# Optimization experiments

Measured on AMD Instinct MI355X. Metric: run time of the kernel, lower is better.

## Reference

```python
import jax, jax.numpy as jnp
import numpy as np
from math import sqrt

BATCH = 32
NUM_CLASSES = 81   # incl. background (class 0 skipped)
MAX_DET = 200      # max_output / per-class NMS candidate cap
IOU_T = 0.5        # criteria in decode_batch_with_nms_trace
CONF_T = 0.05      # score mask threshold


def make_dboxes():
    """Replicates dboxes_R34_coco([1200,1200]) -> (15130, 4) xywh, clipped to [0,1]."""
    fig = 1200
    feat = [50, 25, 13, 7, 3, 3]
    scales = [int(s * fig / 300) for s in [21, 45, 99, 153, 207, 261, 315]]
    ars = [[2], [2, 3], [2, 3], [2, 3], [2], [2]]
    boxes = []
    for idx, f in enumerate(feat):
        sk1 = scales[idx] / fig
        sk2 = scales[idx + 1] / fig
        sk3 = sqrt(sk1 * sk2)
        sizes = [(sk1, sk1), (sk3, sk3)]
        for a in ars[idx]:
            w, h = sk1 * sqrt(a), sk1 / sqrt(a)
            sizes += [(w, h), (h, w)]
        fk = fig // (fig // f)
        for (w, h) in sizes:
            for i in range(f):
                for j in range(f):
                    boxes.append(((j + 0.5) / fk, (i + 0.5) / fk, w, h))
    return np.clip(np.asarray(boxes, np.float32), 0.0, 1.0)


def setup_inputs() -> dict:
    key = jax.random.key(0)
    k1, k2 = jax.random.split(key)
    db = make_dboxes()                      # (15130, 4)
    N = db.shape[0]
    return {
        "bboxes_in": jax.random.normal(k1, (BATCH, 4, N), jnp.float32),
        "scores_in": jax.random.normal(k2, (BATCH, NUM_CLASSES, N), jnp.float32),
        "scale_xy": jnp.full((1,), 0.1, jnp.float32),
        "scale_wh": jnp.full((1,), 0.2, jnp.float32),
        "dboxes_xywh": jnp.asarray(db)[None],  # (1, N, 4)
    }


def _scale_back(bboxes_in, scores_in, scale_xy, scale_wh, dboxes_xywh):
    bb = jnp.transpose(bboxes_in, (0, 2, 1))          # (B, N, 4)
    sc = jnp.transpose(scores_in, (0, 2, 1))          # (B, N, L)
    d_xy, d_wh = dboxes_xywh[..., :2], dboxes_xywh[..., 2:]
    xy = bb[..., :2] * scale_xy * d_wh + d_xy
    wh = jnp.exp(bb[..., 2:] * scale_wh) * d_wh
    ltrb = jnp.concatenate([xy - 0.5 * wh, xy + 0.5 * wh], axis=-1)
    return ltrb, jax.nn.softmax(sc, axis=-1)


def _pairwise_iou(a, b):
    lt = jnp.maximum(a[:, None, :2], b[None, :, :2])
    rb = jnp.minimum(a[:, None, 2:], b[None, :, 2:])
    wh = jnp.clip(rb - lt, 0.0)
    inter = wh[..., 0] * wh[..., 1]
    area_a = (a[:, 2] - a[:, 0]) * (a[:, 3] - a[:, 1])
    area_b = (b[:, 2] - b[:, 0]) * (b[:, 3] - b[:, 1])
    return inter / (area_a[:, None] + area_b[None, :] - inter)


def _nms_one_class(boxes, cls_scores):
    """boxes (N,4), cls_scores (N,) -> (MAX_DET,4), (MAX_DET,) with suppressed = -1."""
    s = jnp.where(cls_scores > CONF_T, cls_scores, -1.0)   # mask score > 0.05
    top_s, idx = jax.lax.top_k(s, MAX_DET)                 # descending topk
    b = boxes[idx]
    iou = _pairwise_iou(b, b)                              # (K, K)
    valid = top_s > CONF_T

    def body(i, keep):  # greedy NMS over score-sorted candidates
        sup = (iou[i] > IOU_T) & keep[i] & (jnp.arange(MAX_DET) > i)
        return keep & ~sup

    keep = jax.lax.stop_gradient(jax.lax.fori_loop(0, MAX_DET, body, valid))
    return b, jnp.where(keep, top_s, -1.0)


def _decode(bboxes_in, scores_in, scale_xy, scale_wh, dboxes_xywh):
    boxes, probs = _scale_back(bboxes_in, scores_in, scale_xy, scale_wh, dboxes_xywh)
    cls_scores = jnp.transpose(probs[..., 1:], (0, 2, 1))   # (B, C=80, N); skip bg
    B, C = cls_scores.shape[0], cls_scores.shape[1]
    per_class = jax.vmap(_nms_one_class, in_axes=(None, 0))
    kb, ks = jax.vmap(per_class, in_axes=(0, 0))(boxes, cls_scores)  # (B,C,K,4),(B,C,K)
    labels = jnp.broadcast_to(
        jnp.arange(1, C + 1, dtype=jnp.int32)[:, None], (C, MAX_DET)).reshape(-1)
    kb = kb.reshape(B, C * MAX_DET, 4)
    ks = ks.reshape(B, C * MAX_DET)
    top_s, top_i = jax.lax.top_k(ks, MAX_DET)               # global top-200
    fb = jnp.take_along_axis(kb, top_i[..., None], axis=1)  # (B, 200, 4)
    fl = labels[top_i]                                      # (B, 200)
    valid = top_s > CONF_T
    return (fb * valid[..., None].astype(fb.dtype),
            jnp.where(valid, fl, 0),
            jnp.where(valid, top_s, 0.0))


def reference(bboxes_in, scores_in, scale_xy, scale_wh, dboxes_xywh):
    return _decode(bboxes_in, scores_in, scale_xy, scale_wh, dboxes_xywh)
```

## Files before the change

### kernel.cpp

```cpp
#include <hip/hip_runtime.h>
#include <stdint.h>

#define NPRIOR   15130
#define BATCH    32
#define NCLS     81
#define NCLS_OUT 80
#define NDET     200
#define CONF_T   0.05f
#define IOU_T    0.5f
#define CAND_CAP 1024
#define NGRP     5
#define GRP      16
#define NCNT     (BATCH * NCLS_OUT)

__global__ __launch_bounds__(256, 1) void decode_softmax_scatter(
    const float* __restrict__ bboxes,
    const float* __restrict__ scores,
    const float* __restrict__ scale_xy_p,
    const float* __restrict__ scale_wh_p,
    const float* __restrict__ dboxes,
    float* __restrict__ boxes_ltrb,
    unsigned int* __restrict__ counters,
    unsigned long long* __restrict__ cand_g)
{
    int b = blockIdx.y;
    int n = blockIdx.x * 256 + threadIdx.x;
    if (n >= NPRIOR) return;

    float sx = scale_xy_p[0], sw = scale_wh_p[0];
    const float* bb = bboxes + (size_t)b * 4 * NPRIOR + n;
    float bx = bb[0];
    float by = bb[NPRIOR];
    float bw = bb[2 * NPRIOR];
    float bh = bb[3 * NPRIOR];
    float4 d = ((const float4*)dboxes)[n];
    float x = __fadd_rn(__fmul_rn(__fmul_rn(bx, sx), d.z), d.x);
    float y = __fadd_rn(__fmul_rn(__fmul_rn(by, sx), d.w), d.y);
    float w = __fmul_rn(expf(__fmul_rn(bw, sw)), d.z);
    float h = __fmul_rn(expf(__fmul_rn(bh, sw)), d.w);
    float hw = __fmul_rn(0.5f, w), hh = __fmul_rn(0.5f, h);
    float4 box;
    box.x = __fsub_rn(x, hw);
    box.y = __fsub_rn(y, hh);
    box.z = __fadd_rn(x, hw);
    box.w = __fadd_rn(y, hh);
    ((float4*)boxes_ltrb)[(size_t)b * NPRIOR + n] = box;

    const float* sc = scores + (size_t)b * NCLS * NPRIOR + n;
    float v[NCLS];
    float mx = -INFINITY;
#pragma unroll
    for (int c = 0; c < NCLS; ++c) {
        v[c] = sc[(size_t)c * NPRIOR];
        mx = fmaxf(mx, v[c]);
    }
    float sum = 0.f;
#pragma unroll
    for (int c = 0; c < NCLS; ++c) {
        v[c] = expf(__fsub_rn(v[c], mx));
        sum = __fadd_rn(sum, v[c]);
    }

    unsigned int invn = 0xFFFFFFFFu - (unsigned int)n;
    unsigned int cbase = (unsigned int)b * NCLS_OUT;
#pragma unroll
    for (int c = 1; c < NCLS; ++c) {
        float p = __fdiv_rn(v[c], sum);
        if (p > CONF_T) {
            unsigned int idx = cbase + (unsigned int)(c - 1);
            unsigned int pos = atomicAdd(&counters[idx], 1u);
            if (pos < CAND_CAP) {
                cand_g[(size_t)idx * CAND_CAP + pos] =
                    ((unsigned long long)__float_as_uint(p) << 32) | (unsigned long long)invn;
            }
        }
    }
}

__device__ inline void bitonic_desc(unsigned long long* keys, int P, int tid) {
    for (int k = 2; k <= P; k <<= 1) {
        for (int j = k >> 1; j > 0; j >>= 1) {
            for (int i = tid; i < P; i += 256) {
                int l = i ^ j;
                if (l > i) {
                    unsigned long long a = keys[i], b = keys[l];
                    bool desc = ((i & k) == 0);
                    if (desc ? (a < b) : (a > b)) {
                        keys[i] = b;
                        keys[l] = a;
                    }
                }
            }
            __syncthreads();
        }
    }
}

__global__ __launch_bounds__(256) void nms_class(
    const unsigned int* __restrict__ counters,
    const unsigned long long* __restrict__ cand_g,
    const float* __restrict__ boxes_ltrb,
    float* __restrict__ cls_scores,
    float* __restrict__ cls_boxes)
{
    __shared__ unsigned long long cand[CAND_CAP];
    __shared__ float sbox[NDET][4];
    __shared__ float sscore[NDET];
    __shared__ unsigned long long rowm[NDET][4];
    __shared__ unsigned long long keepw[4];

    int tid = threadIdx.x;
    int b = blockIdx.y;
    int bc = b * NCLS_OUT + blockIdx.x;

    unsigned int cntu = counters[bc];
    int cnt = (cntu > CAND_CAP) ? CAND_CAP : (int)cntu;

    int P = 256;
    while (P < cnt) P <<= 1;

    for (int i = tid; i < P; i += 256)
        cand[i] = (i < cnt) ? cand_g[(size_t)bc * CAND_CAP + i] : 0ull;
    __syncthreads();

    bitonic_desc(cand, P, tid);

    int m = cnt < NDET ? cnt : NDET;
    if (tid < m) {
        unsigned long long key = cand[tid];
        unsigned int n = 0xFFFFFFFFu - (unsigned int)(key & 0xFFFFFFFFull);
        sscore[tid] = __uint_as_float((unsigned int)(key >> 32));
        float4 bx = ((const float4*)boxes_ltrb)[(size_t)b * NPRIOR + n];
        sbox[tid][0] = bx.x;
        sbox[tid][1] = bx.y;
        sbox[tid][2] = bx.z;
        sbox[tid][3] = bx.w;
    }
    __syncthreads();

    if (tid < m) {
        float l0 = sbox[tid][0], t0 = sbox[tid][1], r0 = sbox[tid][2], b0 = sbox[tid][3];
        float area0 = __fmul_rn(__fsub_rn(r0, l0), __fsub_rn(b0, t0));
        unsigned long long w0 = 0, w1 = 0, w2 = 0, w3 = 0;
        for (int j = tid + 1; j < m; ++j) {
            float lj = sbox[j][0], tj = sbox[j][1], rj = sbox[j][2], bj = sbox[j][3];
            float ltx = fmaxf(l0, lj), lty = fmaxf(t0, tj);
            float rbx = fminf(r0, rj), rby = fminf(b0, bj);
            float iw = fmaxf(__fsub_rn(rbx, ltx), 0.f);
            float ih = fmaxf(__fsub_rn(rby, lty), 0.f);
            float inter = __fmul_rn(iw, ih);
            float areaj = __fmul_rn(__fsub_rn(rj, lj), __fsub_rn(bj, tj));
            float den = __fsub_rn(__fadd_rn(area0, areaj), inter);
            float iou = __fdiv_rn(inter, den);
            if (iou > IOU_T) {
                if (j < 64) w0 |= 1ull << j;
                else if (j < 128) w1 |= 1ull << (j - 64);
                else if (j < 192) w2 |= 1ull << (j - 128);
                else w3 |= 1ull << (j - 192);
            }
        }
        rowm[tid][0] = w0;
        rowm[tid][1] = w1;
        rowm[tid][2] = w2;
        rowm[tid][3] = w3;
    }
    __syncthreads();

    if (tid == 0) {
        auto maskf = [](int t) -> unsigned long long {
            if (t <= 0) return 0ull;
            if (t >= 64) return ~0ull;
            return (1ull << t) - 1ull;
        };
        unsigned long long k0 = maskf(m), k1 = maskf(m - 64), k2 = maskf(m - 128), k3 = maskf(m - 192);
#pragma unroll 4
        for (int i = 0; i < m; ++i) {
            unsigned long long r0 = rowm[i][0], r1 = rowm[i][1];
            unsigned long long r2 = rowm[i][2], r3 = rowm[i][3];
            unsigned long long cur = (i < 64) ? k0 : (i < 128) ? k1 : (i < 192) ? k2 : k3;
            if ((cur >> (i & 63)) & 1ull) {
                k0 &= ~r0; k1 &= ~r1; k2 &= ~r2; k3 &= ~r3;
            }
        }
        keepw[0] = k0; keepw[1] = k1; keepw[2] = k2; keepw[3] = k3;
    }
    __syncthreads();

    if (tid < NDET) {
        float s = -1.0f;
        if (tid < m && ((keepw[tid >> 6] >> (tid & 63)) & 1ull)) s = sscore[tid];
        cls_scores[(size_t)bc * NDET + tid] = s;
        if (tid < m) {
            float4 bx;
            bx.x = sbox[tid][0]; bx.y = sbox[tid][1];
            bx.z = sbox[tid][2]; bx.w = sbox[tid][3];
            ((float4*)cls_boxes)[(size_t)bc * NDET + tid] = bx;
        }
    }
}

__global__ __launch_bounds__(256) void topk_group(
    const float* __restrict__ cls_scores,
    unsigned long long* __restrict__ grp_keys)
{
    __shared__ unsigned long long keys[4096];
    __shared__ unsigned int cnt_s;

    int tid = threadIdx.x;
    int g = blockIdx.x, b = blockIdx.y;
    if (tid == 0) cnt_s = 0;
    __syncthreads();

    int base_e = g * GRP * NDET;
    const float* sp = cls_scores + (size_t)b * NCLS_OUT * NDET + base_e;
    for (int i = tid; i < GRP * NDET; i += 256) {
        float s = sp[i];
        if (s > CONF_T) {
            unsigned int pos = atomicAdd(&cnt_s, 1u);
            unsigned int e = (unsigned int)(base_e + i);
            keys[pos] = ((unsigned long long)__float_as_uint(s) << 32) |
                        (unsigned long long)(0xFFFFFFFFu - e);
        }
    }
    __syncthreads();
    int cnt = (int)cnt_s;
    int P = 256;
    while (P < cnt) P <<= 1;
    for (int i = tid; i < P; i += 256)
        if (i >= cnt) keys[i] = 0ull;
    __syncthreads();

    bitonic_desc(keys, P, tid);

    if (tid < NDET)
        grp_keys[((size_t)b * NGRP + g) * NDET + tid] = (tid < cnt) ? keys[tid] : 0ull;
}

__global__ __launch_bounds__(256) void final_topk(
    const unsigned long long* __restrict__ grp_keys,
    const float* __restrict__ cls_boxes,
    float* __restrict__ out)
{
    __shared__ unsigned long long keys[1024];
    __shared__ unsigned int cnt_s;

    int tid = threadIdx.x, b = blockIdx.x;
    if (tid == 0) cnt_s = 0;
    __syncthreads();

    for (int i = tid; i < NGRP * NDET; i += 256) {
        unsigned long long k = grp_keys[(size_t)b * NGRP * NDET + i];
        if (k != 0ull) keys[atomicAdd(&cnt_s, 1u)] = k;
    }
    __syncthreads();
    int cnt = (int)cnt_s;
    int P = 256;
    while (P < cnt) P <<= 1;
    for (int i = tid; i < P; i += 256)
        if (i >= cnt) keys[i] = 0ull;
    __syncthreads();

    bitonic_desc(keys, P, tid);

    if (tid < NDET) {
        float4 bx = make_float4(0.f, 0.f, 0.f, 0.f);
        float lab = 0.f, sc = 0.f;
        if (tid < cnt) {
            unsigned long long k = keys[tid];
            unsigned int e = 0xFFFFFFFFu - (unsigned int)(k & 0xFFFFFFFFull);
            sc = __uint_as_float((unsigned int)(k >> 32));
            unsigned int c0 = e / NDET;
            bx = ((const float4*)cls_boxes)[(size_t)b * NCLS_OUT * NDET + e];
            lab = (float)(c0 + 1);
        }
        float* fb = out;
        float* fl = out + (size_t)BATCH * NDET * 4;
        float* fs = fl + (size_t)BATCH * NDET;
        ((float4*)fb)[b * NDET + tid] = bx;
        fl[b * NDET + tid] = lab;
        fs[b * NDET + tid] = sc;
    }
}

extern "C" void kernel_launch(void* const* d_in, const int* in_sizes, int n_in,
                              void* d_out, int out_size, void* d_ws, size_t ws_size,
                              hipStream_t stream) {
    const float* bboxes = (const float*)d_in[0];
    const float* scores = (const float*)d_in[1];
    const float* sxy    = (const float*)d_in[2];
    const float* swh    = (const float*)d_in[3];
    const float* dbx    = (const float*)d_in[4];
    float* out = (float*)d_out;

    char* ws = (char*)d_ws;
    size_t off = 0;
    auto alloc = [&](size_t bytes) -> char* {
        char* p = ws + off;
        off += (bytes + 255) & ~(size_t)255;
        return p;
    };
    float* boxes_ltrb            = (float*)alloc((size_t)BATCH * NPRIOR * 4 * 4);
    unsigned int* counters       = (unsigned int*)alloc((size_t)NCNT * 4);
    unsigned long long* cand_g   = (unsigned long long*)alloc((size_t)NCNT * CAND_CAP * 8);
    float* cls_scores            = (float*)alloc((size_t)BATCH * NCLS_OUT * NDET * 4);
    float* cls_boxes             = (float*)alloc((size_t)BATCH * NCLS_OUT * NDET * 4 * 4);
    unsigned long long* grp_keys = (unsigned long long*)alloc((size_t)BATCH * NGRP * NDET * 8);

    hipMemsetAsync(counters, 0, (size_t)NCNT * 4, stream);

    dim3 gridA((NPRIOR + 255) / 256, BATCH);
    decode_softmax_scatter<<<gridA, 256, 0, stream>>>(
        bboxes, scores, sxy, swh, dbx, boxes_ltrb, counters, cand_g);

    dim3 gridB(NCLS_OUT, BATCH);
    nms_class<<<gridB, 256, 0, stream>>>(counters, cand_g, boxes_ltrb, cls_scores, cls_boxes);

    dim3 gridC1(NGRP, BATCH);
    topk_group<<<gridC1, 256, 0, stream>>>(cls_scores, grp_keys);

    final_topk<<<BATCH, 256, 0, stream>>>(grp_keys, cls_boxes, out);
}
```

Baseline: 812.9 us.

## Split softmax across thread pairs, elide bitonic syncs, parallelize NMS keep scan

The decode/softmax kernel now gives each prior to two threads, each handling about half of the 81 classes. The threads exchange the max and the sum with shuffles, and the original summation order is kept. This roughly halves the per-thread register array, and launch bounds are raised so more waves fit per CU and hide the latency of the strided score loads. The bitonic sort skips __syncthreads for strides below 64, relying on those partners sitting in the same wavefront. The serial single-thread NMS keep scan now runs on one wave, with the mask words held in four lanes, broadcast by shuffle and the next row prefetched. Box storage moves to float4 in shared memory.

```diff
diff --git a/kernel.cpp b/kernel.cpp
--- a/kernel.cpp
+++ b/kernel.cpp
@@ -13,7 +13,7 @@
 #define GRP      16
 #define NCNT     (BATCH * NCLS_OUT)
 
-__global__ __launch_bounds__(256, 1) void decode_softmax_scatter(
+__global__ __launch_bounds__(256, 4) void decode_softmax_scatter(
     const float* __restrict__ bboxes,
     const float* __restrict__ scores,
     const float* __restrict__ scale_xy_p,
@@ -23,63 +23,94 @@
     unsigned int* __restrict__ counters,
     unsigned long long* __restrict__ cand_g)
 {
+    int tid = threadIdx.x;
     int b = blockIdx.y;
-    int n = blockIdx.x * 256 + threadIdx.x;
+    int t = tid & 1;
+    int n = blockIdx.x * 128 + (tid >> 1);
     if (n >= NPRIOR) return;
 
-    float sx = scale_xy_p[0], sw = scale_wh_p[0];
-    const float* bb = bboxes + (size_t)b * 4 * NPRIOR + n;
-    float bx = bb[0];
-    float by = bb[NPRIOR];
-    float bw = bb[2 * NPRIOR];
-    float bh = bb[3 * NPRIOR];
-    float4 d = ((const float4*)dboxes)[n];
-    float x = __fadd_rn(__fmul_rn(__fmul_rn(bx, sx), d.z), d.x);
-    float y = __fadd_rn(__fmul_rn(__fmul_rn(by, sx), d.w), d.y);
-    float w = __fmul_rn(expf(__fmul_rn(bw, sw)), d.z);
-    float h = __fmul_rn(expf(__fmul_rn(bh, sw)), d.w);
-    float hw = __fmul_rn(0.5f, w), hh = __fmul_rn(0.5f, h);
-    float4 box;
-    box.x = __fsub_rn(x, hw);
-    box.y = __fsub_rn(y, hh);
-    box.z = __fadd_rn(x, hw);
-    box.w = __fadd_rn(y, hh);
-    ((float4*)boxes_ltrb)[(size_t)b * NPRIOR + n] = box;
-
-    const float* sc = scores + (size_t)b * NCLS * NPRIOR + n;
-    float v[NCLS];
+    if (t == 0) {
+        float sx = scale_xy_p[0], sw = scale_wh_p[0];
+        const float* bb = bboxes + (size_t)b * 4 * NPRIOR + n;
+        float bx = bb[0];
+        float by = bb[NPRIOR];
+        float bw = bb[2 * NPRIOR];
+        float bh = bb[3 * NPRIOR];
+        float4 d = ((const float4*)dboxes)[n];
+        float x = __fadd_rn(__fmul_rn(__fmul_rn(bx, sx), d.z), d.x);
+        float y = __fadd_rn(__fmul_rn(__fmul_rn(by, sx), d.w), d.y);
+        float w = __fmul_rn(expf(__fmul_rn(bw, sw)), d.z);
+        float h = __fmul_rn(expf(__fmul_rn(bh, sw)), d.w);
+        float hw = __fmul_rn(0.5f, w), hh = __fmul_rn(0.5f, h);
+        float4 box;
+        box.x = __fsub_rn(x, hw);
+        box.y = __fsub_rn(y, hh);
+        box.z = __fadd_rn(x, hw);
+        box.w = __fadd_rn(y, hh);
+        ((float4*)boxes_ltrb)[(size_t)b * NPRIOR + n] = box;
+    }
+
+    int cls0 = t * 41;
+    const float* sc = scores + ((size_t)b * NCLS + cls0) * NPRIOR + n;
+    float v[41];
     float mx = -INFINITY;
 #pragma unroll
-    for (int c = 0; c < NCLS; ++c) {
-        v[c] = sc[(size_t)c * NPRIOR];
-        mx = fmaxf(mx, v[c]);
-    }
-    float sum = 0.f;
-#pragma unroll
-    for (int c = 0; c < NCLS; ++c) {
-        v[c] = expf(__fsub_rn(v[c], mx));
-        sum = __fadd_rn(sum, v[c]);
-    }
+    for (int k = 0; k < 41; ++k) {
+        if (k < 40 || t == 0) {
+            v[k] = sc[(size_t)k * NPRIOR];
+            mx = fmaxf(mx, v[k]);
+        }
+    }
+    mx = fmaxf(mx, __shfl_xor(mx, 1));
+
+#pragma unroll
+    for (int k = 0; k < 41; ++k)
+        if (k < 40 || t == 0)
+            v[k] = expf(__fsub_rn(v[k], mx));
+
+    float s = 0.f;
+    if (t == 0) {
+#pragma unroll
+        for (int k = 0; k < 41; ++k) s = __fadd_rn(s, v[k]);
+    }
+    float se = __shfl_xor(s, 1);
+    float total = 0.f;
+    if (t == 1) {
+        float acc = se;
+#pragma unroll
+        for (int k = 0; k < 40; ++k) acc = __fadd_rn(acc, v[k]);
+        total = acc;
+    }
+    float tot_other = __shfl_xor(total, 1);
+    float sum = (t == 1) ? total : tot_other;
 
     unsigned int invn = 0xFFFFFFFFu - (unsigned int)n;
     unsigned int cbase = (unsigned int)b * NCLS_OUT;
 #pragma unroll
-    for (int c = 1; c < NCLS; ++c) {
-        float p = __fdiv_rn(v[c], sum);
-        if (p > CONF_T) {
-            unsigned int idx = cbase + (unsigned int)(c - 1);
-            unsigned int pos = atomicAdd(&counters[idx], 1u);
-            if (pos < CAND_CAP) {
-                cand_g[(size_t)idx * CAND_CAP + pos] =
-                    ((unsigned long long)__float_as_uint(p) << 32) | (unsigned long long)invn;
+    for (int k = 0; k < 41; ++k) {
+        if (k < 40 || t == 0) {
+            int cls = cls0 + k;
+            if (cls > 0) {
+                float p = __fdiv_rn(v[k], sum);
+                if (p > CONF_T) {
+                    unsigned int idx = cbase + (unsigned int)(cls - 1);
+                    unsigned int pos = atomicAdd(&counters[idx], 1u);
+                    if (pos < CAND_CAP) {
+                        cand_g[(size_t)idx * CAND_CAP + pos] =
+                            ((unsigned long long)__float_as_uint(p) << 32) |
+                            (unsigned long long)invn;
+                    }
+                }
             }
         }
     }
 }
 
 __device__ inline void bitonic_desc(unsigned long long* keys, int P, int tid) {
+    int prevj = 64;
     for (int k = 2; k <= P; k <<= 1) {
         for (int j = k >> 1; j > 0; j >>= 1) {
+            if (j >= 64 || prevj >= 64) __syncthreads();
             for (int i = tid; i < P; i += 256) {
                 int l = i ^ j;
                 if (l > i) {
@@ -91,7 +122,7 @@
                     }
                 }
             }
-            __syncthreads();
+            prevj = j;
         }
     }
 }
@@ -104,7 +135,7 @@
     float* __restrict__ cls_boxes)
 {
     __shared__ unsigned long long cand[CAND_CAP];
-    __shared__ float sbox[NDET][4];
+    __shared__ float4 sbox4[NDET];
     __shared__ float sscore[NDET];
     __shared__ unsigned long long rowm[NDET][4];
     __shared__ unsigned long long keepw[4];
@@ -121,7 +152,6 @@
 
     for (int i = tid; i < P; i += 256)
         cand[i] = (i < cnt) ? cand_g[(size_t)bc * CAND_CAP + i] : 0ull;
-    __syncthreads();
 
     bitonic_desc(cand, P, tid);
 
@@ -130,26 +160,22 @@
         unsigned long long key = cand[tid];
         unsigned int n = 0xFFFFFFFFu - (unsigned int)(key & 0xFFFFFFFFull);
         sscore[tid] = __uint_as_float((unsigned int)(key >> 32));
-        float4 bx = ((const float4*)boxes_ltrb)[(size_t)b * NPRIOR + n];
-        sbox[tid][0] = bx.x;
-        sbox[tid][1] = bx.y;
-        sbox[tid][2] = bx.z;
-        sbox[tid][3] = bx.w;
+        sbox4[tid] = ((const float4*)boxes_ltrb)[(size_t)b * NPRIOR + n];
     }
     __syncthreads();
 
     if (tid < m) {
-        float l0 = sbox[tid][0], t0 = sbox[tid][1], r0 = sbox[tid][2], b0 = sbox[tid][3];
-        float area0 = __fmul_rn(__fsub_rn(r0, l0), __fsub_rn(b0, t0));
+        float4 bi = sbox4[tid];
+        float area0 = __fmul_rn(__fsub_rn(bi.z, bi.x), __fsub_rn(bi.w, bi.y));
         unsigned long long w0 = 0, w1 = 0, w2 = 0, w3 = 0;
         for (int j = tid + 1; j < m; ++j) {
-            float lj = sbox[j][0], tj = sbox[j][1], rj = sbox[j][2], bj = sbox[j][3];
-            float ltx = fmaxf(l0, lj), lty = fmaxf(t0, tj);
-            float rbx = fminf(r0, rj), rby = fminf(b0, bj);
+            float4 bj = sbox4[j];
+            float ltx = fmaxf(bi.x, bj.x), lty = fmaxf(bi.y, bj.y);
+            float rbx = fminf(bi.z, bj.z), rby = fminf(bi.w, bj.w);
             float iw = fmaxf(__fsub_rn(rbx, ltx), 0.f);
             float ih = fmaxf(__fsub_rn(rby, lty), 0.f);
             float inter = __fmul_rn(iw, ih);
-            float areaj = __fmul_rn(__fsub_rn(rj, lj), __fsub_rn(bj, tj));
+            float areaj = __fmul_rn(__fsub_rn(bj.z, bj.x), __fsub_rn(bj.w, bj.y));
             float den = __fsub_rn(__fadd_rn(area0, areaj), inter);
             float iou = __fdiv_rn(inter, den);
             if (iou > IOU_T) {
@@ -166,23 +192,23 @@
     }
     __syncthreads();
 
-    if (tid == 0) {
-        auto maskf = [](int t) -> unsigned long long {
-            if (t <= 0) return 0ull;
-            if (t >= 64) return ~0ull;
-            return (1ull << t) - 1ull;
-        };
-        unsigned long long k0 = maskf(m), k1 = maskf(m - 64), k2 = maskf(m - 128), k3 = maskf(m - 192);
-#pragma unroll 4
+    if (tid < 64) {
+        int lane = tid;
+        unsigned long long kreg = 0ull;
+        if (lane < 4) {
+            int rem = m - lane * 64;
+            kreg = (rem >= 64) ? ~0ull : (rem <= 0 ? 0ull : ((1ull << rem) - 1ull));
+        }
+        unsigned long long cur = (lane < 4 && m > 0) ? rowm[0][lane] : 0ull;
         for (int i = 0; i < m; ++i) {
-            unsigned long long r0 = rowm[i][0], r1 = rowm[i][1];
-            unsigned long long r2 = rowm[i][2], r3 = rowm[i][3];
-            unsigned long long cur = (i < 64) ? k0 : (i < 128) ? k1 : (i < 192) ? k2 : k3;
-            if ((cur >> (i & 63)) & 1ull) {
-                k0 &= ~r0; k1 &= ~r1; k2 &= ~r2; k3 &= ~r3;
+            unsigned long long nxt = (lane < 4 && (i + 1) < m) ? rowm[i + 1][lane] : 0ull;
+            unsigned long long kw = __shfl(kreg, i >> 6);
+            if ((kw >> (i & 63)) & 1ull) {
+                if (lane < 4) kreg &= ~cur;
             }
-        }
-        keepw[0] = k0; keepw[1] = k1; keepw[2] = k2; keepw[3] = k3;
+            cur = nxt;
+        }
+        if (lane < 4) keepw[lane] = kreg;
     }
     __syncthreads();
 
@@ -190,12 +216,8 @@
         float s = -1.0f;
         if (tid < m && ((keepw[tid >> 6] >> (tid & 63)) & 1ull)) s = sscore[tid];
         cls_scores[(size_t)bc * NDET + tid] = s;
-        if (tid < m) {
-            float4 bx;
-            bx.x = sbox[tid][0]; bx.y = sbox[tid][1];
-            bx.z = sbox[tid][2]; bx.w = sbox[tid][3];
-            ((float4*)cls_boxes)[(size_t)bc * NDET + tid] = bx;
-        }
+        if (tid < m)
+            ((float4*)cls_boxes)[(size_t)bc * NDET + tid] = sbox4[tid];
     }
 }
 
@@ -228,7 +250,6 @@
     while (P < cnt) P <<= 1;
     for (int i = tid; i < P; i += 256)
         if (i >= cnt) keys[i] = 0ull;
-    __syncthreads();
 
     bitonic_desc(keys, P, tid);
 
@@ -258,7 +279,6 @@
     while (P < cnt) P <<= 1;
     for (int i = tid; i < P; i += 256)
         if (i >= cnt) keys[i] = 0ull;
-    __syncthreads();
 
     bitonic_desc(keys, P, tid);
 
@@ -308,7 +328,7 @@
 
     hipMemsetAsync(counters, 0, (size_t)NCNT * 4, stream);
 
-    dim3 gridA((NPRIOR + 255) / 256, BATCH);
+    dim3 gridA((NPRIOR + 127) / 128, BATCH);
     decode_softmax_scatter<<<gridA, 256, 0, stream>>>(
         bboxes, scores, sxy, swh, dbx, boxes_ltrb, counters, cand_g);
 
```

Result: slower. 997.4 us (+22.7%).
